# Kernel optimization log

Measured on AMD Instinct MI355X. Metric: run time of the kernel, lower is better.

## Reference

```python
import jax, jax.numpy as jnp
import numpy as np

DIM = 1024
SCALE = 1.0 / np.sqrt(DIM).astype(np.float32)


def setup_inputs() -> dict:
    key = jax.random.key(0)
    ks = jax.random.split(key, 8)
    B, S, D = 4, 2048, DIM
    x = jax.random.normal(ks[0], (B, S, D), dtype=jnp.float32)
    mask = jnp.zeros((S, S), dtype=jnp.float32)  # additive mask, broadcast over batch
    # learned params (nn.Linear: y = x @ W.T + b); store W already transposed for x @ W
    init = 1.0 / np.sqrt(D)
    Wq = jax.random.uniform(ks[1], (D, D), jnp.float32, -init, init)
    bq = jax.random.uniform(ks[2], (D,), jnp.float32, -init, init)
    Wk = jax.random.uniform(ks[3], (D, D), jnp.float32, -init, init)
    bk = jax.random.uniform(ks[4], (D,), jnp.float32, -init, init)
    Wv = jax.random.uniform(ks[5], (D, D), jnp.float32, -init, init)
    bv = jax.random.uniform(ks[6], (D,), jnp.float32, -init, init)
    return {"x": x, "mask": mask, "Wq": Wq, "bq": bq, "Wk": Wk, "bk": bk, "Wv": Wv, "bv": bv}


def reference(x, mask, Wq, bq, Wk, bk, Wv, bv):
    # single-head full-dim attention, scaled by 1/sqrt(dim) (as in the source)
    q = x @ Wq + bq                      # [B, S, D]
    k = x @ Wk + bk                      # [B, S, D]
    v = x @ Wv + bv                      # [B, S, D]
    scores = jnp.einsum('bqd,bkd->bqk', q, k) * SCALE  # [B, S, S]
    scores = scores + mask               # additive mask, broadcast
    attn = jax.nn.softmax(scores, axis=-1)
    # dropout(p=0.1) is identity in eval mode
    return jnp.einsum('bqk,bkd->bqd', attn, v)  # [B, S, D]
```

## Files before the change

### kernel.cpp

```cpp
#include <hip/hip_runtime.h>

typedef unsigned short u16;
typedef unsigned int u32;

typedef __attribute__((ext_vector_type(8))) short bf16x8;
typedef __attribute__((ext_vector_type(4))) float f32x4;

static __device__ __forceinline__ u16 f2bf(float f) {
    u32 u = __float_as_uint(f);
    u32 r = (u + 0x7FFFu + ((u >> 16) & 1u)) >> 16;
    return (u16)r;
}
static __device__ __forceinline__ float bf2f(u16 h) {
    return __uint_as_float(((u32)h) << 16);
}
static __device__ __forceinline__ u32 pack2(float a, float b) {
    return (u32)f2bf(a) | ((u32)f2bf(b) << 16);
}

__global__ __launch_bounds__(256) void convert_bf16_kernel(const float* __restrict__ x,
                                                           u16* __restrict__ y, int n4) {
    int i = blockIdx.x * 256 + threadIdx.x;
    if (i < n4) {
        float4 v = ((const float4*)x)[i];
        ushort4 o;
        o.x = f2bf(v.x); o.y = f2bf(v.y); o.z = f2bf(v.z); o.w = f2bf(v.w);
        ((ushort4*)y)[i] = o;
    }
}

__global__ __launch_bounds__(256) void transpose3_to_bf16_kernel(
    const float* __restrict__ W0, const float* __restrict__ W1, const float* __restrict__ W2,
    u16* __restrict__ T0, u16* __restrict__ T1, u16* __restrict__ T2, int D) {
    __shared__ float t[32][33];
    const float* W = (blockIdx.z == 0) ? W0 : (blockIdx.z == 1) ? W1 : W2;
    u16* WT = (blockIdx.z == 0) ? T0 : (blockIdx.z == 1) ? T1 : T2;
    int bx = blockIdx.x, by = blockIdx.y;
    int tx = threadIdx.x, ty = threadIdx.y;
#pragma unroll
    for (int i = ty; i < 32; i += 8)
        t[i][tx] = W[(long)(by * 32 + i) * D + bx * 32 + tx];
    __syncthreads();
#pragma unroll
    for (int i = ty; i < 32; i += 8)
        WT[(long)(bx * 32 + i) * D + by * 32 + tx] = f2bf(t[tx][i]);
}

__global__ __launch_bounds__(256) void concat_bias_kernel(const float* __restrict__ a,
                                                          const float* __restrict__ b,
                                                          float* __restrict__ o, int n) {
    int i = blockIdx.x * 256 + threadIdx.x;
    if (i < 2 * n) o[i] = (i < n) ? a[i] : b[i - n];
}

__global__ __launch_bounds__(512, 2) void gemm256_kernel(
    const u16* __restrict__ A, int lda, long sA,
    const u16* __restrict__ B, int ldb, long sB,
    void* __restrict__ C, int ldc, long sC, int c_bf16,
    const float* __restrict__ bias, int bias_mode,
    const float* __restrict__ madd, int mask_ld,
    float* __restrict__ rowsum, int rs_mode, int rs_ld,
    float scale, int K) {
    __shared__ __align__(16) u16 SMEM[2][2 * 256 * 64];
    const int bz = blockIdx.z;
    const u16* Ab = A + (long)bz * sA;
    const u16* Bb = B + (long)bz * sB;
    int bx, by;
    {
        const int gx = gridDim.x;
        int flat = blockIdx.y * gx + blockIdx.x;
        const int cpx = (gx * gridDim.y) >> 3;
        flat = (flat & 7) * cpx + (flat >> 3);
        bx = flat % gx;
        by = flat / gx;
    }
    const int tm = by << 8, tn = bx << 8;
    const int tid = threadIdx.x, wave = tid >> 6, lane = tid & 63;
    const int wq = wave & 3;
    const int wm = (wave >> 2) << 7;
    const int wn = wq << 6;
    const int fm = lane & 15, fq = lane >> 4;
    const int T = K >> 6;

    f32x4 acc[8][4];
#pragma unroll
    for (int i = 0; i < 8; i++)
#pragma unroll
        for (int j = 0; j < 4; j++) acc[i][j] = (f32x4){0.f, 0.f, 0.f, 0.f};

    const int srow = tid >> 3;
    const int sslot = tid & 7;

    auto stageA = [&](int t, int half) {
        u16* dst = &SMEM[t & 1][0];
        const int kb = t << 6;
#pragma unroll
        for (int blk = 0; blk < 2; blk++) {
            const int r0 = blk * 128 + half * 64;
            const int r = r0 + srow;
            const int gk = kb + ((sslot ^ (r & 7)) << 3);
            const u16* ga = Ab + (long)(tm + r) * lda + gk;
            __builtin_amdgcn_global_load_lds(
                (const __attribute__((address_space(1))) void*)ga,
                (__attribute__((address_space(3))) void*)&dst[(r0 + wave * 8) * 64], 16, 0, 0);
        }
    };
    auto stageB = [&](int t, int half) {
        u16* dst = &SMEM[t & 1][256 * 64];
        const int kb = t << 6;
#pragma unroll
        for (int blk = 0; blk < 2; blk++) {
            const int r0 = half * 128 + blk * 64;
            const int r = r0 + srow;
            const int g = ((r >> 5) & 3) * 64 + (r >> 7) * 32 + (r & 31);
            const int gk = kb + ((sslot ^ (r & 7)) << 3);
            const u16* gb = Bb + (long)(tn + g) * ldb + gk;
            __builtin_amdgcn_global_load_lds(
                (const __attribute__((address_space(1))) void*)gb,
                (__attribute__((address_space(3))) void*)&dst[(r0 + wave * 8) * 64], 16, 0, 0);
        }
    };

    auto read_a4 = [&](const u16* Ls, bf16x8 (&d)[4][2], int base) {
#pragma unroll
        for (int i = 0; i < 4; i++) {
            const int ra = base + i * 16 + fm;
            const int sw = ra & 7;
#pragma unroll
            for (int kh = 0; kh < 2; kh++)
                d[i][kh] = *(const bf16x8*)&Ls[ra * 64 + (((kh * 4 + fq) ^ sw) << 3)];
        }
    };
    auto read_b2 = [&](const u16* Ls, bf16x8 (&d)[2][2], int base) {
#pragma unroll
        for (int j = 0; j < 2; j++) {
            const int rb = base + j * 16 + fm;
            const int sw = rb & 7;
#pragma unroll
            for (int kh = 0; kh < 2; kh++)
                d[j][kh] = *(const bf16x8*)&Ls[rb * 64 + (((kh * 4 + fq) ^ sw) << 3)];
        }
    };

    stageA(0, 0); stageB(0, 0); stageA(0, 1); stageB(0, 1);
    if (T > 1) {
        stageA(1, 0); stageB(1, 0); stageA(1, 1);
        asm volatile("s_waitcnt vmcnt(6)" ::: "memory");
    } else {
        asm volatile("s_waitcnt vmcnt(0)" ::: "memory");
    }
    __builtin_amdgcn_sched_barrier(0);
    __builtin_amdgcn_s_barrier();
    __builtin_amdgcn_sched_barrier(0);

    bf16x8 alo[4][2], ahi[4][2], blo[2][2], bhi[2][2];
    read_a4(&SMEM[0][0], alo, wm);
    read_b2(&SMEM[0][256 * 64], blo, wq * 32);

    for (int u = 0; u < T; ++u) {
        const u16* As = &SMEM[u & 1][0];
        const u16* Bs = &SMEM[u & 1][256 * 64];
        const u16* As2 = &SMEM[(u + 1) & 1][0];
        const u16* Bs2 = &SMEM[(u + 1) & 1][256 * 64];
        if (u + 1 < T) stageB(u + 1, 1);
        read_b2(Bs, bhi, 128 + wq * 32);
        __builtin_amdgcn_sched_barrier(0);
        __builtin_amdgcn_s_setprio(1);
#pragma unroll
        for (int kh = 0; kh < 2; kh++)
#pragma unroll
            for (int i = 0; i < 4; i++)
#pragma unroll
                for (int j = 0; j < 2; j++)
                    acc[i][j] = __builtin_amdgcn_mfma_f32_16x16x32_bf16(alo[i][kh], blo[j][kh], acc[i][j], 0, 0, 0);
        __builtin_amdgcn_s_setprio(0);
        __builtin_amdgcn_sched_barrier(0);
        __builtin_amdgcn_s_barrier();
        __builtin_amdgcn_sched_barrier(0);
        if (u + 2 < T) stageA(u + 2, 0);
        read_a4(As, ahi, wm + 64);
        __builtin_amdgcn_sched_barrier(0);
        __builtin_amdgcn_s_setprio(1);
#pragma unroll
        for (int kh = 0; kh < 2; kh++)
#pragma unroll
            for (int i = 0; i < 4; i++)
#pragma unroll
                for (int j = 0; j < 2; j++)
                    acc[i][2 + j] = __builtin_amdgcn_mfma_f32_16x16x32_bf16(alo[i][kh], bhi[j][kh], acc[i][2 + j], 0, 0, 0);
        __builtin_amdgcn_s_setprio(0);
        __builtin_amdgcn_sched_barrier(0);
        __builtin_amdgcn_s_barrier();
        __builtin_amdgcn_sched_barrier(0);
        if (u + 2 < T) stageB(u + 2, 0);
        __builtin_amdgcn_sched_barrier(0);
        __builtin_amdgcn_s_setprio(1);
#pragma unroll
        for (int kh = 0; kh < 2; kh++)
#pragma unroll
            for (int i = 0; i < 4; i++)
#pragma unroll
                for (int j = 0; j < 2; j++)
                    acc[4 + i][j] = __builtin_amdgcn_mfma_f32_16x16x32_bf16(ahi[i][kh], blo[j][kh], acc[4 + i][j], 0, 0, 0);
        __builtin_amdgcn_s_setprio(0);
        __builtin_amdgcn_sched_barrier(0);
        __builtin_amdgcn_s_barrier();
        __builtin_amdgcn_sched_barrier(0);
        if (u + 2 < T) {
            stageA(u + 2, 1);
            asm volatile("s_waitcnt vmcnt(6)" ::: "memory");
        } else {
            asm volatile("s_waitcnt vmcnt(0)" ::: "memory");
        }
        __builtin_amdgcn_sched_barrier(0);
        __builtin_amdgcn_s_barrier();
        __builtin_amdgcn_sched_barrier(0);
        if (u + 1 < T) {
            read_a4(As2, alo, wm);
            read_b2(Bs2, blo, wq * 32);
        }
        __builtin_amdgcn_sched_barrier(0);
        __builtin_amdgcn_s_setprio(1);
#pragma unroll
        for (int kh = 0; kh < 2; kh++)
#pragma unroll
            for (int i = 0; i < 4; i++)
#pragma unroll
                for (int j = 0; j < 2; j++)
                    acc[4 + i][2 + j] = __builtin_amdgcn_mfma_f32_16x16x32_bf16(ahi[i][kh], bhi[j][kh], acc[4 + i][2 + j], 0, 0, 0);
        __builtin_amdgcn_s_setprio(0);
    }
    __syncthreads();

    float* EP = (float*)&SMEM[0][0] + wave * 1088;
    const int row16 = lane >> 2, cb = (lane & 3) * 16;
    float4 bc[4];
    if (bias_mode == 1) {
#pragma unroll
        for (int q = 0; q < 4; q++) bc[q] = *(const float4*)&bias[tn + wn + cb + q * 4];
    }
#pragma unroll
    for (int i = 0; i < 8; i++) {
#pragma unroll
        for (int j = 0; j < 4; j++)
#pragma unroll
            for (int r = 0; r < 4; r++)
                EP[(fq * 4 + r) * 68 + j * 16 + fm] = acc[i][j][r];
        const long grow = tm + wm + i * 16 + row16;
        float rb = (bias_mode == 2) ? bias[grow] : 0.f;
        float4 t4[4];
#pragma unroll
        for (int q = 0; q < 4; q++) {
            float4 v = *(const float4*)&EP[row16 * 68 + cb + q * 4];
            v.x = v.x * scale + rb; v.y = v.y * scale + rb;
            v.z = v.z * scale + rb; v.w = v.w * scale + rb;
            if (bias_mode == 1) { v.x += bc[q].x; v.y += bc[q].y; v.z += bc[q].z; v.w += bc[q].w; }
            if (madd) {
                float4 m4 = *(const float4*)&madd[grow * mask_ld + tn + wn + cb + q * 4];
                v.x += m4.x; v.y += m4.y; v.z += m4.z; v.w += m4.w;
            }
            t4[q] = v;
        }
        if (rs_mode == 1) {
            float s = 0.f;
#pragma unroll
            for (int q = 0; q < 4; q++) {
                t4[q].x = __expf(t4[q].x); t4[q].y = __expf(t4[q].y);
                t4[q].z = __expf(t4[q].z); t4[q].w = __expf(t4[q].w);
                s += t4[q].x + t4[q].y + t4[q].z + t4[q].w;
            }
            s += __shfl_xor(s, 1);
            s += __shfl_xor(s, 2);
            if ((lane & 3) == 0) atomicAdd(&rowsum[(long)bz * rs_ld + grow], s);
        } else if (rs_mode == 2) {
            float inv = 1.f / rowsum[(long)bz * rs_ld + grow];
#pragma unroll
            for (int q = 0; q < 4; q++) {
                t4[q].x *= inv; t4[q].y *= inv; t4[q].z *= inv; t4[q].w *= inv;
            }
        }
        if (c_bf16) {
            u16* dst = (u16*)C + (long)bz * sC + grow * ldc + tn + wn + cb;
            uint4 o0 = {pack2(t4[0].x, t4[0].y), pack2(t4[0].z, t4[0].w),
                        pack2(t4[1].x, t4[1].y), pack2(t4[1].z, t4[1].w)};
            uint4 o1 = {pack2(t4[2].x, t4[2].y), pack2(t4[2].z, t4[2].w),
                        pack2(t4[3].x, t4[3].y), pack2(t4[3].z, t4[3].w)};
            *(uint4*)dst = o0;
            *(uint4*)(dst + 8) = o1;
        } else {
            float* dst = (float*)C + (long)bz * sC + grow * ldc + tn + wn + cb;
#pragma unroll
            for (int q = 0; q < 4; q++) *(float4*)(dst + q * 4) = t4[q];
        }
    }
}

__global__ __launch_bounds__(256, 4) void gemm_bt_kernel(
    const u16* __restrict__ A, int lda, long sA,
    const u16* __restrict__ B, int ldb, long sB,
    void* __restrict__ C, int ldc, long sC, int c_bf16,
    const float* __restrict__ bias, int bias_mode,
    const float* __restrict__ madd, int mask_ld,
    float* __restrict__ rowsum, int rs_mode, int rs_ld, int swapxy,
    float scale, int K) {
    __shared__ __align__(16) u16 SMEM[2][256 * 32];
    const int bz = blockIdx.z;
    const u16* Ab = A + (long)bz * sA;
    const u16* Bb = B + (long)bz * sB;
    const int bxi = swapxy ? blockIdx.y : blockIdx.x;
    const int byi = swapxy ? blockIdx.x : blockIdx.y;
    const int tm = byi * 128, tn = bxi * 128;
    const int tid = threadIdx.x, wave = tid >> 6, lane = tid & 63;
    const int wm = (wave >> 1) * 64, wn = (wave & 1) * 64;
    const int lr = lane >> 2, c = lane & 3;
    const int fm = lane & 15, fq = lane >> 4;

    f32x4 acc[4][4];
#pragma unroll
    for (int i = 0; i < 4; i++)
#pragma unroll
        for (int j = 0; j < 4; j++) acc[i][j] = (f32x4){0.f, 0.f, 0.f, 0.f};

    const int T = K >> 5;

    auto stage = [&](int t, int buf) {
        u16* As = &SMEM[buf][0];
        u16* Bs = &SMEM[buf][128 * 32];
#pragma unroll
        for (int r = 0; r < 2; r++) {
            const int rl = r * 64 + wave * 16;
            const int row = rl + lr;
            const int kc = (t << 5) + ((c ^ ((row ^ (row >> 2)) & 3)) << 3);
            const u16* ga = Ab + (long)(tm + row) * lda + kc;
            const u16* gb = Bb + (long)(tn + row) * ldb + kc;
            __builtin_amdgcn_global_load_lds((const __attribute__((address_space(1))) void*)ga,
                                             (__attribute__((address_space(3))) void*)&As[rl * 32],
                                             16, 0, 0);
            __builtin_amdgcn_global_load_lds((const __attribute__((address_space(1))) void*)gb,
                                             (__attribute__((address_space(3))) void*)&Bs[rl * 32],
                                             16, 0, 0);
        }
    };

    stage(0, 0);
    __syncthreads();
    for (int t = 0; t < T; t++) {
        const int cur = t & 1;
        if (t + 1 < T) stage(t + 1, cur ^ 1);
        const u16* As = &SMEM[cur][0];
        const u16* Bs = &SMEM[cur][128 * 32];
        bf16x8 af[4], bfr[4];
#pragma unroll
        for (int i = 0; i < 4; i++) {
            int row = wm + i * 16 + fm;
            af[i] = *(const bf16x8*)&As[row * 32 + ((fq ^ ((row ^ (row >> 2)) & 3)) << 3)];
        }
#pragma unroll
        for (int j = 0; j < 4; j++) {
            int row = wn + j * 16 + fm;
            bfr[j] = *(const bf16x8*)&Bs[row * 32 + ((fq ^ ((row ^ (row >> 2)) & 3)) << 3)];
        }
#pragma unroll
        for (int i = 0; i < 4; i++)
#pragma unroll
            for (int j = 0; j < 4; j++)
                acc[i][j] = __builtin_amdgcn_mfma_f32_16x16x32_bf16(af[i], bfr[j], acc[i][j], 0, 0, 0);
        if (t + 1 < T) __syncthreads();
    }
    __syncthreads();

    float* EP = (float*)&SMEM[0][0] + wave * 1088;
    const int row16 = lane >> 2, cb = (lane & 3) * 16;
    float4 bc[4];
    if (bias_mode == 1) {
#pragma unroll
        for (int q = 0; q < 4; q++) bc[q] = *(const float4*)&bias[tn + wn + cb + q * 4];
    }
#pragma unroll
    for (int i = 0; i < 4; i++) {
#pragma unroll
        for (int j = 0; j < 4; j++)
#pragma unroll
            for (int r = 0; r < 4; r++)
                EP[(fq * 4 + r) * 68 + j * 16 + fm] = acc[i][j][r];
        const long grow = tm + wm + i * 16 + row16;
        float rb = (bias_mode == 2) ? bias[grow] : 0.f;
        float4 t4[4];
#pragma unroll
        for (int q = 0; q < 4; q++) {
            float4 v = *(const float4*)&EP[row16 * 68 + cb + q * 4];
            v.x = v.x * scale + rb; v.y = v.y * scale + rb;
            v.z = v.z * scale + rb; v.w = v.w * scale + rb;
            if (bias_mode == 1) { v.x += bc[q].x; v.y += bc[q].y; v.z += bc[q].z; v.w += bc[q].w; }
            if (madd) {
                float4 m4 = *(const float4*)&madd[grow * mask_ld + tn + wn + cb + q * 4];
                v.x += m4.x; v.y += m4.y; v.z += m4.z; v.w += m4.w;
            }
            t4[q] = v;
        }
        if (rs_mode == 1) {
            float s = 0.f;
#pragma unroll
            for (int q = 0; q < 4; q++) {
                t4[q].x = __expf(t4[q].x); t4[q].y = __expf(t4[q].y);
                t4[q].z = __expf(t4[q].z); t4[q].w = __expf(t4[q].w);
                s += t4[q].x + t4[q].y + t4[q].z + t4[q].w;
            }
            s += __shfl_xor(s, 1);
            s += __shfl_xor(s, 2);
            if ((lane & 3) == 0) atomicAdd(&rowsum[(long)bz * rs_ld + grow], s);
        } else if (rs_mode == 2) {
            float inv = 1.f / rowsum[(long)bz * rs_ld + grow];
#pragma unroll
            for (int q = 0; q < 4; q++) {
                t4[q].x *= inv; t4[q].y *= inv; t4[q].z *= inv; t4[q].w *= inv;
            }
        }
        if (c_bf16) {
            u16* dst = (u16*)C + (long)bz * sC + grow * ldc + tn + wn + cb;
            uint4 o0 = {pack2(t4[0].x, t4[0].y), pack2(t4[0].z, t4[0].w),
                        pack2(t4[1].x, t4[1].y), pack2(t4[1].z, t4[1].w)};
            uint4 o1 = {pack2(t4[2].x, t4[2].y), pack2(t4[2].z, t4[2].w),
                        pack2(t4[3].x, t4[3].y), pack2(t4[3].z, t4[3].w)};
            *(uint4*)dst = o0;
            *(uint4*)(dst + 8) = o1;
        } else {
            float* dst = (float*)C + (long)bz * sC + grow * ldc + tn + wn + cb;
#pragma unroll
            for (int q = 0; q < 4; q++) *(float4*)(dst + q * 4) = t4[q];
        }
    }
}

extern "C" void kernel_launch(void* const* d_in, const int* in_sizes, int n_in,
                              void* d_out, int out_size, void* d_ws, size_t ws_size,
                              hipStream_t stream) {
    const float* x    = (const float*)d_in[0];
    const float* mask = (const float*)d_in[1];
    const float* Wq   = (const float*)d_in[2];
    const float* bq   = (const float*)d_in[3];
    const float* Wk   = (const float*)d_in[4];
    const float* bk   = (const float*)d_in[5];
    const float* Wv   = (const float*)d_in[6];
    const float* bv   = (const float*)d_in[7];
    float* out = (float*)d_out;

    const int B = 4, S = 2048, D = 1024;
    const long MS = (long)B * S;

    size_t need = (size_t)MS * D * 2 + (size_t)(2 * D) * D * 2 + (size_t)D * D * 2
                + (size_t)(2 * D) * 4 + (size_t)MS * (2 * D) * 2 + (size_t)D * MS * 2
                + (size_t)B * S * S * 2 + (size_t)B * S * 4;
    if (ws_size < need) return;

    char* ws = (char*)d_ws;
    u16*  xb   = (u16*)ws;  ws += (long)MS * D * 2;
    u16*  wqkt = (u16*)ws;  ws += (long)(2 * D) * D * 2;
    u16*  wvt  = (u16*)ws;  ws += (long)D * D * 2;
    float* bqk = (float*)ws; ws += (long)(2 * D) * 4;
    u16*  QK   = (u16*)ws;  ws += (long)MS * (2 * D) * 2;
    u16*  VT   = (u16*)ws;  ws += (long)D * MS * 2;
    u16*  sc   = (u16*)ws;  ws += (long)B * S * S * 2;
    float* rsum = (float*)ws; ws += (long)B * S * 4;

    const float SCALE = 0.03125f;

    hipMemsetAsync(rsum, 0, (size_t)B * S * 4, stream);

    convert_bf16_kernel<<<(int)((MS * D / 4 + 255) / 256), 256, 0, stream>>>(x, xb, (int)(MS * D / 4));
    transpose3_to_bf16_kernel<<<dim3(32, 32, 3), dim3(32, 8), 0, stream>>>(
        Wq, Wk, Wv, wqkt, wqkt + (long)D * D, wvt, D);
    concat_bias_kernel<<<8, 256, 0, stream>>>(bq, bk, bqk, D);

    gemm256_kernel<<<dim3(2 * D / 256, (int)(MS / 256), 1), 512, 0, stream>>>(
        xb, D, 0, wqkt, D, 0, QK, 2 * D, 0, 1, bqk, 1, nullptr, 0,
        nullptr, 0, 0, 1.0f, D);
    gemm_bt_kernel<<<dim3((int)(MS / 128), D / 128, 1), 256, 0, stream>>>(
        wvt, D, 0, xb, D, 0, VT, (int)MS, 0, 1, bv, 2, nullptr, 0,
        nullptr, 0, 0, 0, 1.0f, D);

    gemm256_kernel<<<dim3(S / 256, S / 256, B), 512, 0, stream>>>(
        QK, 2 * D, (long)S * 2 * D, QK + D, 2 * D, (long)S * 2 * D, sc, S, (long)S * S, 1,
        nullptr, 0, mask, S, rsum, 1, S, SCALE, D);

    gemm_bt_kernel<<<dim3(S / 128, D / 128, B), 256, 0, stream>>>(
        sc, S, (long)S * S, VT, (int)MS, (long)S, out, D, (long)S * D, 0,
        nullptr, 0, nullptr, 0, rsum, 2, S, 1, 1.0f, S);
}
```

Measured before the change: 279.0 us.

## Store the attention mask as bf16 and remap PV GEMM blocks per XCD

The additive mask is converted once to bf16 in a new small kernel. The score GEMM epilogue then reads half as many mask bytes for each of the four batches. The P·V GEMM grid is reshaped so that blockIdx.x selects the XCD, and each XCD handles one half of one batch, to keep that batch's score rows and V^T in a single L2. The cost is an extra conversion pass over the mask and bf16 rounding of mask values, which changes results for masks that bf16 cannot represent exactly.

```diff
diff --git a/kernel.cpp b/kernel.cpp
--- a/kernel.cpp
+++ b/kernel.cpp
@@ -58,7 +58,7 @@
     const u16* __restrict__ B, int ldb, long sB,
     void* __restrict__ C, int ldc, long sC, int c_bf16,
     const float* __restrict__ bias, int bias_mode,
-    const float* __restrict__ madd, int mask_ld,
+    const u16* __restrict__ madd, int mask_ld,
     float* __restrict__ rowsum, int rs_mode, int rs_ld,
     float scale, int K) {
     __shared__ __align__(16) u16 SMEM[2][2 * 256 * 64];
@@ -256,8 +256,8 @@
             v.z = v.z * scale + rb; v.w = v.w * scale + rb;
             if (bias_mode == 1) { v.x += bc[q].x; v.y += bc[q].y; v.z += bc[q].z; v.w += bc[q].w; }
             if (madd) {
-                float4 m4 = *(const float4*)&madd[grow * mask_ld + tn + wn + cb + q * 4];
-                v.x += m4.x; v.y += m4.y; v.z += m4.z; v.w += m4.w;
+                ushort4 m4 = *(const ushort4*)&madd[grow * mask_ld + tn + wn + cb + q * 4];
+                v.x += bf2f(m4.x); v.y += bf2f(m4.y); v.z += bf2f(m4.z); v.w += bf2f(m4.w);
             }
             t4[q] = v;
         }
@@ -301,14 +301,22 @@
     void* __restrict__ C, int ldc, long sC, int c_bf16,
     const float* __restrict__ bias, int bias_mode,
     const float* __restrict__ madd, int mask_ld,
-    float* __restrict__ rowsum, int rs_mode, int rs_ld, int swapxy,
+    float* __restrict__ rowsum, int rs_mode, int rs_ld, int xcd_mode,
     float scale, int K) {
     __shared__ __align__(16) u16 SMEM[2][256 * 32];
-    const int bz = blockIdx.z;
+    int bxi, byi, bzi;
+    if (xcd_mode == 1) {
+        const int xcd = blockIdx.x;
+        const int s = blockIdx.y + (gridDim.y * blockIdx.z);
+        bzi = xcd >> 1;
+        byi = (xcd & 1) * 8 + (s >> 3);
+        bxi = s & 7;
+    } else {
+        bxi = blockIdx.x; byi = blockIdx.y; bzi = blockIdx.z;
+    }
+    const int bz = bzi;
     const u16* Ab = A + (long)bz * sA;
     const u16* Bb = B + (long)bz * sB;
-    const int bxi = swapxy ? blockIdx.y : blockIdx.x;
-    const int byi = swapxy ? blockIdx.x : blockIdx.y;
     const int tm = byi * 128, tn = bxi * 128;
     const int tid = threadIdx.x, wave = tid >> 6, lane = tid & 63;
     const int wm = (wave >> 1) * 64, wn = (wave & 1) * 64;
@@ -450,7 +458,7 @@
 
     size_t need = (size_t)MS * D * 2 + (size_t)(2 * D) * D * 2 + (size_t)D * D * 2
                 + (size_t)(2 * D) * 4 + (size_t)MS * (2 * D) * 2 + (size_t)D * MS * 2
-                + (size_t)B * S * S * 2 + (size_t)B * S * 4;
+                + (size_t)B * S * S * 2 + (size_t)B * S * 4 + (size_t)S * S * 2;
     if (ws_size < need) return;
 
     char* ws = (char*)d_ws;
@@ -462,12 +470,15 @@
     u16*  VT   = (u16*)ws;  ws += (long)D * MS * 2;
     u16*  sc   = (u16*)ws;  ws += (long)B * S * S * 2;
     float* rsum = (float*)ws; ws += (long)B * S * 4;
+    u16*  maskb = (u16*)ws; ws += (long)S * S * 2;
 
     const float SCALE = 0.03125f;
 
     hipMemsetAsync(rsum, 0, (size_t)B * S * 4, stream);
 
     convert_bf16_kernel<<<(int)((MS * D / 4 + 255) / 256), 256, 0, stream>>>(x, xb, (int)(MS * D / 4));
+    convert_bf16_kernel<<<(int)(((long)S * S / 4 + 255) / 256), 256, 0, stream>>>(
+        mask, maskb, (int)((long)S * S / 4));
     transpose3_to_bf16_kernel<<<dim3(32, 32, 3), dim3(32, 8), 0, stream>>>(
         Wq, Wk, Wv, wqkt, wqkt + (long)D * D, wvt, D);
     concat_bias_kernel<<<8, 256, 0, stream>>>(bq, bk, bqk, D);
@@ -481,9 +492,9 @@
 
     gemm256_kernel<<<dim3(S / 256, S / 256, B), 512, 0, stream>>>(
         QK, 2 * D, (long)S * 2 * D, QK + D, 2 * D, (long)S * 2 * D, sc, S, (long)S * S, 1,
-        nullptr, 0, mask, S, rsum, 1, S, SCALE, D);
-
-    gemm_bt_kernel<<<dim3(S / 128, D / 128, B), 256, 0, stream>>>(
+        nullptr, 0, maskb, S, rsum, 1, S, SCALE, D);
+
+    gemm_bt_kernel<<<dim3(D / 128, S / 128, B), 256, 0, stream>>>(
         sc, S, (long)S * S, VT, (int)MS, (long)S, out, D, (long)S * D, 0,
         nullptr, 0, nullptr, 0, rsum, 2, S, 1, 1.0f, S);
 }
```

New measurement: 281.6 us. No clear change (+0.9%).

## Merge prep and QKV projection launches, bf16 mask, specialize attention GEMMs

Applied to the files above, without the earlier changes.

Folds the x conversion, weight transposes and bias concat into one prep kernel. The Q/K projection and V^T projection run in a single launch that also converts the mask to bf16 and zeroes the row sums, with the QK projection moving from 256-tiles to a shared 128-tile core. The score GEMM now reads the bf16 mask instead of fp32 and drops its runtime mode branches, and the PV GEMM is specialized with an XCD-aware block remap. This cuts launch count and mask traffic, but adds mask rounding to bf16 and a smaller tile for the QK projection.

```diff
diff --git a/kernel.cpp b/kernel.cpp
--- a/kernel.cpp
+++ b/kernel.cpp
@@ -18,48 +18,178 @@
     return (u32)f2bf(a) | ((u32)f2bf(b) << 16);
 }
 
-__global__ __launch_bounds__(256) void convert_bf16_kernel(const float* __restrict__ x,
-                                                           u16* __restrict__ y, int n4) {
-    int i = blockIdx.x * 256 + threadIdx.x;
-    if (i < n4) {
+__global__ __launch_bounds__(256) void prep_kernel(
+    const float* __restrict__ x, u16* __restrict__ xb,
+    const float* __restrict__ Wq, const float* __restrict__ Wk, const float* __restrict__ Wv,
+    u16* __restrict__ T0, u16* __restrict__ T1, u16* __restrict__ T2,
+    const float* __restrict__ bq, const float* __restrict__ bk,
+    float* __restrict__ bqk) {
+    const int D = 1024;
+    int bid = blockIdx.x;
+    const int tid = threadIdx.x;
+    if (bid < 8192) {
+        long i = (long)bid * 256 + tid;
         float4 v = ((const float4*)x)[i];
-        ushort4 o;
-        o.x = f2bf(v.x); o.y = f2bf(v.y); o.z = f2bf(v.z); o.w = f2bf(v.w);
-        ((ushort4*)y)[i] = o;
-    }
-}
-
-__global__ __launch_bounds__(256) void transpose3_to_bf16_kernel(
-    const float* __restrict__ W0, const float* __restrict__ W1, const float* __restrict__ W2,
-    u16* __restrict__ T0, u16* __restrict__ T1, u16* __restrict__ T2, int D) {
-    __shared__ float t[32][33];
-    const float* W = (blockIdx.z == 0) ? W0 : (blockIdx.z == 1) ? W1 : W2;
-    u16* WT = (blockIdx.z == 0) ? T0 : (blockIdx.z == 1) ? T1 : T2;
-    int bx = blockIdx.x, by = blockIdx.y;
-    int tx = threadIdx.x, ty = threadIdx.y;
-#pragma unroll
-    for (int i = ty; i < 32; i += 8)
-        t[i][tx] = W[(long)(by * 32 + i) * D + bx * 32 + tx];
+        ushort4 o; o.x = f2bf(v.x); o.y = f2bf(v.y); o.z = f2bf(v.z); o.w = f2bf(v.w);
+        ((ushort4*)xb)[i] = o;
+        return;
+    }
+    bid -= 8192;
+    if (bid < 3072) {
+        __shared__ float t[32][33];
+        const int z = bid >> 10, loc = bid & 1023;
+        const int bx = loc & 31, by = loc >> 5;
+        const float* W = (z == 0) ? Wq : (z == 1) ? Wk : Wv;
+        u16* WT = (z == 0) ? T0 : (z == 1) ? T1 : T2;
+        const int tx = tid & 31, ty = tid >> 5;
+#pragma unroll
+        for (int i = ty; i < 32; i += 8)
+            t[i][tx] = W[(long)(by * 32 + i) * D + bx * 32 + tx];
+        __syncthreads();
+#pragma unroll
+        for (int i = ty; i < 32; i += 8)
+            WT[(long)(bx * 32 + i) * D + by * 32 + tx] = f2bf(t[tx][i]);
+        return;
+    }
+    bid -= 3072;
+    {
+        int i = bid * 256 + tid;
+        bqk[i] = (i < 1024) ? bq[i] : bk[i - 1024];
+    }
+}
+
+static __device__ __forceinline__ void gemm_core(
+    u16* __restrict__ SM,
+    const u16* __restrict__ Ab, int lda,
+    const u16* __restrict__ Bb, int ldb,
+    void* __restrict__ Cb, int ldc, int c_bf16,
+    const float* __restrict__ bias, int bias_mode,
+    float scale, int K, int tm, int tn) {
+    const int tid = threadIdx.x, wave = tid >> 6, lane = tid & 63;
+    const int wm = (wave >> 1) * 64, wn = (wave & 1) * 64;
+    const int lr = lane >> 2, c = lane & 3;
+    const int fm = lane & 15, fq = lane >> 4;
+
+    f32x4 acc[4][4];
+#pragma unroll
+    for (int i = 0; i < 4; i++)
+#pragma unroll
+        for (int j = 0; j < 4; j++) acc[i][j] = (f32x4){0.f, 0.f, 0.f, 0.f};
+
+    const int T = K >> 5;
+
+    auto stage = [&](int t, int buf) {
+        u16* As = SM + buf * 8192;
+        u16* Bs = As + 4096;
+#pragma unroll
+        for (int r = 0; r < 2; r++) {
+            const int rl = r * 64 + wave * 16;
+            const int row = rl + lr;
+            const int kc = (t << 5) + ((c ^ ((row ^ (row >> 2)) & 3)) << 3);
+            const u16* ga = Ab + (long)(tm + row) * lda + kc;
+            const u16* gb = Bb + (long)(tn + row) * ldb + kc;
+            __builtin_amdgcn_global_load_lds((const __attribute__((address_space(1))) void*)ga,
+                                             (__attribute__((address_space(3))) void*)&As[rl * 32],
+                                             16, 0, 0);
+            __builtin_amdgcn_global_load_lds((const __attribute__((address_space(1))) void*)gb,
+                                             (__attribute__((address_space(3))) void*)&Bs[rl * 32],
+                                             16, 0, 0);
+        }
+    };
+
+    stage(0, 0);
     __syncthreads();
-#pragma unroll
-    for (int i = ty; i < 32; i += 8)
-        WT[(long)(bx * 32 + i) * D + by * 32 + tx] = f2bf(t[tx][i]);
-}
-
-__global__ __launch_bounds__(256) void concat_bias_kernel(const float* __restrict__ a,
-                                                          const float* __restrict__ b,
-                                                          float* __restrict__ o, int n) {
-    int i = blockIdx.x * 256 + threadIdx.x;
-    if (i < 2 * n) o[i] = (i < n) ? a[i] : b[i - n];
+    for (int t = 0; t < T; t++) {
+        const int cur = t & 1;
+        if (t + 1 < T) stage(t + 1, cur ^ 1);
+        const u16* As = SM + cur * 8192;
+        const u16* Bs = As + 4096;
+        bf16x8 af[4], bfr[4];
+#pragma unroll
+        for (int i = 0; i < 4; i++) {
+            int row = wm + i * 16 + fm;
+            af[i] = *(const bf16x8*)&As[row * 32 + ((fq ^ ((row ^ (row >> 2)) & 3)) << 3)];
+        }
+#pragma unroll
+        for (int j = 0; j < 4; j++) {
+            int row = wn + j * 16 + fm;
+            bfr[j] = *(const bf16x8*)&Bs[row * 32 + ((fq ^ ((row ^ (row >> 2)) & 3)) << 3)];
+        }
+#pragma unroll
+        for (int i = 0; i < 4; i++)
+#pragma unroll
+            for (int j = 0; j < 4; j++)
+                acc[i][j] = __builtin_amdgcn_mfma_f32_16x16x32_bf16(af[i], bfr[j], acc[i][j], 0, 0, 0);
+        if (t + 1 < T) __syncthreads();
+    }
+    __syncthreads();
+
+    float* EP = (float*)SM + wave * 1088;
+    const int row16 = lane >> 2, cb = (lane & 3) * 16;
+    float4 bc[4];
+    if (bias_mode == 1) {
+#pragma unroll
+        for (int q = 0; q < 4; q++) bc[q] = *(const float4*)&bias[tn + wn + cb + q * 4];
+    }
+#pragma unroll
+    for (int i = 0; i < 4; i++) {
+#pragma unroll
+        for (int j = 0; j < 4; j++)
+#pragma unroll
+            for (int r = 0; r < 4; r++)
+                EP[(fq * 4 + r) * 68 + j * 16 + fm] = acc[i][j][r];
+        const long grow = tm + wm + i * 16 + row16;
+        float rb = (bias_mode == 2) ? bias[grow] : 0.f;
+        float4 t4[4];
+#pragma unroll
+        for (int q = 0; q < 4; q++) {
+            float4 v = *(const float4*)&EP[row16 * 68 + cb + q * 4];
+            v.x = v.x * scale + rb; v.y = v.y * scale + rb;
+            v.z = v.z * scale + rb; v.w = v.w * scale + rb;
+            if (bias_mode == 1) { v.x += bc[q].x; v.y += bc[q].y; v.z += bc[q].z; v.w += bc[q].w; }
+            t4[q] = v;
+        }
+        u16* dst = (u16*)Cb + grow * ldc + tn + wn + cb;
+        uint4 o0 = {pack2(t4[0].x, t4[0].y), pack2(t4[0].z, t4[0].w),
+                    pack2(t4[1].x, t4[1].y), pack2(t4[1].z, t4[1].w)};
+        uint4 o1 = {pack2(t4[2].x, t4[2].y), pack2(t4[2].z, t4[2].w),
+                    pack2(t4[3].x, t4[3].y), pack2(t4[3].z, t4[3].w)};
+        *(uint4*)dst = o0;
+        *(uint4*)(dst + 8) = o1;
+    }
+}
+
+__global__ __launch_bounds__(256, 4) void gemm_qkvt_kernel(
+    const u16* __restrict__ xb, const u16* __restrict__ wqkt, const u16* __restrict__ wvt,
+    u16* __restrict__ QK, u16* __restrict__ VT,
+    const float* __restrict__ bqk, const float* __restrict__ bv,
+    const float* __restrict__ mask, u16* __restrict__ maskb, float* __restrict__ rsum) {
+    __shared__ __align__(16) u16 SM[2][256 * 32];
+    const int D = 1024, MS = 8192;
+    const int id = blockIdx.x;
+    if (id < 1024) {
+        gemm_core(&SM[0][0], xb, D, wqkt, D, QK, 2 * D, 1, bqk, 1,
+                  1.0f, D, (id >> 4) * 128, (id & 15) * 128);
+    } else if (id < 1536) {
+        const int f = id - 1024;
+        gemm_core(&SM[0][0], wvt, D, xb, D, VT, MS, 1, bv, 2,
+                  1.0f, D, (f >> 6) * 128, (f & 63) * 128);
+    } else if (id < 5632) {
+        long i = (long)(id - 1536) * 256 + threadIdx.x;
+        float4 v = ((const float4*)mask)[i];
+        ushort4 o; o.x = f2bf(v.x); o.y = f2bf(v.y); o.z = f2bf(v.z); o.w = f2bf(v.w);
+        ((ushort4*)maskb)[i] = o;
+    } else {
+        rsum[(id - 5632) * 256 + threadIdx.x] = 0.f;
+    }
 }
 
 __global__ __launch_bounds__(512, 2) void gemm256_kernel(
     const u16* __restrict__ A, int lda, long sA,
     const u16* __restrict__ B, int ldb, long sB,
-    void* __restrict__ C, int ldc, long sC, int c_bf16,
-    const float* __restrict__ bias, int bias_mode,
-    const float* __restrict__ madd, int mask_ld,
-    float* __restrict__ rowsum, int rs_mode, int rs_ld,
+    void* __restrict__ C, int ldc, long sC,
+    const u16* __restrict__ madd, int mask_ld,
+    float* __restrict__ rowsum, int rs_ld,
     float scale, int K) {
     __shared__ __align__(16) u16 SMEM[2][2 * 256 * 64];
     const int bz = blockIdx.z;
@@ -234,11 +364,6 @@
 
     float* EP = (float*)&SMEM[0][0] + wave * 1088;
     const int row16 = lane >> 2, cb = (lane & 3) * 16;
-    float4 bc[4];
-    if (bias_mode == 1) {
-#pragma unroll
-        for (int q = 0; q < 4; q++) bc[q] = *(const float4*)&bias[tn + wn + cb + q * 4];
-    }
 #pragma unroll
     for (int i = 0; i < 8; i++) {
 #pragma unroll
@@ -247,68 +372,48 @@
             for (int r = 0; r < 4; r++)
                 EP[(fq * 4 + r) * 68 + j * 16 + fm] = acc[i][j][r];
         const long grow = tm + wm + i * 16 + row16;
-        float rb = (bias_mode == 2) ? bias[grow] : 0.f;
         float4 t4[4];
 #pragma unroll
         for (int q = 0; q < 4; q++) {
             float4 v = *(const float4*)&EP[row16 * 68 + cb + q * 4];
-            v.x = v.x * scale + rb; v.y = v.y * scale + rb;
-            v.z = v.z * scale + rb; v.w = v.w * scale + rb;
-            if (bias_mode == 1) { v.x += bc[q].x; v.y += bc[q].y; v.z += bc[q].z; v.w += bc[q].w; }
-            if (madd) {
-                float4 m4 = *(const float4*)&madd[grow * mask_ld + tn + wn + cb + q * 4];
-                v.x += m4.x; v.y += m4.y; v.z += m4.z; v.w += m4.w;
-            }
+            ushort4 m4 = *(const ushort4*)&madd[grow * mask_ld + tn + wn + cb + q * 4];
+            v.x = v.x * scale + bf2f(m4.x); v.y = v.y * scale + bf2f(m4.y);
+            v.z = v.z * scale + bf2f(m4.z); v.w = v.w * scale + bf2f(m4.w);
             t4[q] = v;
         }
-        if (rs_mode == 1) {
-            float s = 0.f;
-#pragma unroll
-            for (int q = 0; q < 4; q++) {
-                t4[q].x = __expf(t4[q].x); t4[q].y = __expf(t4[q].y);
-                t4[q].z = __expf(t4[q].z); t4[q].w = __expf(t4[q].w);
-                s += t4[q].x + t4[q].y + t4[q].z + t4[q].w;
-            }
-            s += __shfl_xor(s, 1);
-            s += __shfl_xor(s, 2);
-            if ((lane & 3) == 0) atomicAdd(&rowsum[(long)bz * rs_ld + grow], s);
-        } else if (rs_mode == 2) {
-            float inv = 1.f / rowsum[(long)bz * rs_ld + grow];
-#pragma unroll
-            for (int q = 0; q < 4; q++) {
-                t4[q].x *= inv; t4[q].y *= inv; t4[q].z *= inv; t4[q].w *= inv;
-            }
-        }
-        if (c_bf16) {
-            u16* dst = (u16*)C + (long)bz * sC + grow * ldc + tn + wn + cb;
-            uint4 o0 = {pack2(t4[0].x, t4[0].y), pack2(t4[0].z, t4[0].w),
-                        pack2(t4[1].x, t4[1].y), pack2(t4[1].z, t4[1].w)};
-            uint4 o1 = {pack2(t4[2].x, t4[2].y), pack2(t4[2].z, t4[2].w),
-                        pack2(t4[3].x, t4[3].y), pack2(t4[3].z, t4[3].w)};
-            *(uint4*)dst = o0;
-            *(uint4*)(dst + 8) = o1;
-        } else {
-            float* dst = (float*)C + (long)bz * sC + grow * ldc + tn + wn + cb;
-#pragma unroll
-            for (int q = 0; q < 4; q++) *(float4*)(dst + q * 4) = t4[q];
-        }
-    }
-}
-
-__global__ __launch_bounds__(256, 4) void gemm_bt_kernel(
-    const u16* __restrict__ A, int lda, long sA,
-    const u16* __restrict__ B, int ldb, long sB,
-    void* __restrict__ C, int ldc, long sC, int c_bf16,
-    const float* __restrict__ bias, int bias_mode,
-    const float* __restrict__ madd, int mask_ld,
-    float* __restrict__ rowsum, int rs_mode, int rs_ld, int swapxy,
-    float scale, int K) {
+        float s = 0.f;
+#pragma unroll
+        for (int q = 0; q < 4; q++) {
+            t4[q].x = __expf(t4[q].x); t4[q].y = __expf(t4[q].y);
+            t4[q].z = __expf(t4[q].z); t4[q].w = __expf(t4[q].w);
+            s += t4[q].x + t4[q].y + t4[q].z + t4[q].w;
+        }
+        s += __shfl_xor(s, 1);
+        s += __shfl_xor(s, 2);
+        if ((lane & 3) == 0) atomicAdd(&rowsum[(long)bz * rs_ld + grow], s);
+        u16* dst = (u16*)C + (long)bz * sC + grow * ldc + tn + wn + cb;
+        uint4 o0 = {pack2(t4[0].x, t4[0].y), pack2(t4[0].z, t4[0].w),
+                    pack2(t4[1].x, t4[1].y), pack2(t4[1].z, t4[1].w)};
+        uint4 o1 = {pack2(t4[2].x, t4[2].y), pack2(t4[2].z, t4[2].w),
+                    pack2(t4[3].x, t4[3].y), pack2(t4[3].z, t4[3].w)};
+        *(uint4*)dst = o0;
+        *(uint4*)(dst + 8) = o1;
+    }
+}
+
+__global__ __launch_bounds__(256, 4) void gemm_pv_kernel(
+    const u16* __restrict__ sc, const u16* __restrict__ VT,
+    float* __restrict__ out, const float* __restrict__ rsum) {
     __shared__ __align__(16) u16 SMEM[2][256 * 32];
-    const int bz = blockIdx.z;
-    const u16* Ab = A + (long)bz * sA;
-    const u16* Bb = B + (long)bz * sB;
-    const int bxi = swapxy ? blockIdx.y : blockIdx.x;
-    const int byi = swapxy ? blockIdx.x : blockIdx.y;
+    const int S = 2048, D = 1024, MS = 8192;
+    const int xcd = blockIdx.x;
+    const int s = blockIdx.y + gridDim.y * blockIdx.z;
+    const int bz = xcd >> 1;
+    const int byi = (xcd & 1) * 8 + (s >> 3);
+    const int bxi = s & 7;
+    const u16* Ab = sc + (long)bz * S * S;
+    const u16* Bb = VT + (long)bz * S;
+    const float* rs = rsum + (long)bz * S;
     const int tm = byi * 128, tn = bxi * 128;
     const int tid = threadIdx.x, wave = tid >> 6, lane = tid & 63;
     const int wm = (wave >> 1) * 64, wn = (wave & 1) * 64;
@@ -321,7 +426,7 @@
 #pragma unroll
         for (int j = 0; j < 4; j++) acc[i][j] = (f32x4){0.f, 0.f, 0.f, 0.f};
 
-    const int T = K >> 5;
+    const int T = S >> 5;
 
     auto stage = [&](int t, int buf) {
         u16* As = &SMEM[buf][0];
@@ -331,8 +436,8 @@
             const int rl = r * 64 + wave * 16;
             const int row = rl + lr;
             const int kc = (t << 5) + ((c ^ ((row ^ (row >> 2)) & 3)) << 3);
-            const u16* ga = Ab + (long)(tm + row) * lda + kc;
-            const u16* gb = Bb + (long)(tn + row) * ldb + kc;
+            const u16* ga = Ab + (long)(tm + row) * S + kc;
+            const u16* gb = Bb + (long)(tn + row) * MS + kc;
             __builtin_amdgcn_global_load_lds((const __attribute__((address_space(1))) void*)ga,
                                              (__attribute__((address_space(3))) void*)&As[rl * 32],
                                              16, 0, 0);
@@ -371,11 +476,6 @@
 
     float* EP = (float*)&SMEM[0][0] + wave * 1088;
     const int row16 = lane >> 2, cb = (lane & 3) * 16;
-    float4 bc[4];
-    if (bias_mode == 1) {
-#pragma unroll
-        for (int q = 0; q < 4; q++) bc[q] = *(const float4*)&bias[tn + wn + cb + q * 4];
-    }
 #pragma unroll
     for (int i = 0; i < 4; i++) {
 #pragma unroll
@@ -384,50 +484,13 @@
             for (int r = 0; r < 4; r++)
                 EP[(fq * 4 + r) * 68 + j * 16 + fm] = acc[i][j][r];
         const long grow = tm + wm + i * 16 + row16;
-        float rb = (bias_mode == 2) ? bias[grow] : 0.f;
-        float4 t4[4];
+        float inv = 1.f / rs[grow];
+        float* dst = out + (long)bz * S * D + grow * D + tn + wn + cb;
 #pragma unroll
         for (int q = 0; q < 4; q++) {
             float4 v = *(const float4*)&EP[row16 * 68 + cb + q * 4];
-            v.x = v.x * scale + rb; v.y = v.y * scale + rb;
-            v.z = v.z * scale + rb; v.w = v.w * scale + rb;
-            if (bias_mode == 1) { v.x += bc[q].x; v.y += bc[q].y; v.z += bc[q].z; v.w += bc[q].w; }
-            if (madd) {
-                float4 m4 = *(const float4*)&madd[grow * mask_ld + tn + wn + cb + q * 4];
-                v.x += m4.x; v.y += m4.y; v.z += m4.z; v.w += m4.w;
-            }
-            t4[q] = v;
-        }
-        if (rs_mode == 1) {
-            float s = 0.f;
-#pragma unroll
-            for (int q = 0; q < 4; q++) {
-                t4[q].x = __expf(t4[q].x); t4[q].y = __expf(t4[q].y);
-                t4[q].z = __expf(t4[q].z); t4[q].w = __expf(t4[q].w);
-                s += t4[q].x + t4[q].y + t4[q].z + t4[q].w;
-            }
-            s += __shfl_xor(s, 1);
-            s += __shfl_xor(s, 2);
-            if ((lane & 3) == 0) atomicAdd(&rowsum[(long)bz * rs_ld + grow], s);
-        } else if (rs_mode == 2) {
-            float inv = 1.f / rowsum[(long)bz * rs_ld + grow];
-#pragma unroll
-            for (int q = 0; q < 4; q++) {
-                t4[q].x *= inv; t4[q].y *= inv; t4[q].z *= inv; t4[q].w *= inv;
-            }
-        }
-        if (c_bf16) {
-            u16* dst = (u16*)C + (long)bz * sC + grow * ldc + tn + wn + cb;
-            uint4 o0 = {pack2(t4[0].x, t4[0].y), pack2(t4[0].z, t4[0].w),
-                        pack2(t4[1].x, t4[1].y), pack2(t4[1].z, t4[1].w)};
-            uint4 o1 = {pack2(t4[2].x, t4[2].y), pack2(t4[2].z, t4[2].w),
-                        pack2(t4[3].x, t4[3].y), pack2(t4[3].z, t4[3].w)};
-            *(uint4*)dst = o0;
-            *(uint4*)(dst + 8) = o1;
-        } else {
-            float* dst = (float*)C + (long)bz * sC + grow * ldc + tn + wn + cb;
-#pragma unroll
-            for (int q = 0; q < 4; q++) *(float4*)(dst + q * 4) = t4[q];
+            v.x *= inv; v.y *= inv; v.z *= inv; v.w *= inv;
+            *(float4*)(dst + q * 4) = v;
         }
     }
 }
@@ -450,7 +513,7 @@
 
     size_t need = (size_t)MS * D * 2 + (size_t)(2 * D) * D * 2 + (size_t)D * D * 2
                 + (size_t)(2 * D) * 4 + (size_t)MS * (2 * D) * 2 + (size_t)D * MS * 2
-                + (size_t)B * S * S * 2 + (size_t)B * S * 4;
+                + (size_t)B * S * S * 2 + (size_t)B * S * 4 + (size_t)S * S * 2;
     if (ws_size < need) return;
 
     char* ws = (char*)d_ws;
@@ -462,28 +525,16 @@
     u16*  VT   = (u16*)ws;  ws += (long)D * MS * 2;
     u16*  sc   = (u16*)ws;  ws += (long)B * S * S * 2;
     float* rsum = (float*)ws; ws += (long)B * S * 4;
+    u16*  maskb = (u16*)ws; ws += (long)S * S * 2;
 
     const float SCALE = 0.03125f;
 
-    hipMemsetAsync(rsum, 0, (size_t)B * S * 4, stream);
-
-    convert_bf16_kernel<<<(int)((MS * D / 4 + 255) / 256), 256, 0, stream>>>(x, xb, (int)(MS * D / 4));
-    transpose3_to_bf16_kernel<<<dim3(32, 32, 3), dim3(32, 8), 0, stream>>>(
-        Wq, Wk, Wv, wqkt, wqkt + (long)D * D, wvt, D);
-    concat_bias_kernel<<<8, 256, 0, stream>>>(bq, bk, bqk, D);
-
-    gemm256_kernel<<<dim3(2 * D / 256, (int)(MS / 256), 1), 512, 0, stream>>>(
-        xb, D, 0, wqkt, D, 0, QK, 2 * D, 0, 1, bqk, 1, nullptr, 0,
-        nullptr, 0, 0, 1.0f, D);
-    gemm_bt_kernel<<<dim3((int)(MS / 128), D / 128, 1), 256, 0, stream>>>(
-        wvt, D, 0, xb, D, 0, VT, (int)MS, 0, 1, bv, 2, nullptr, 0,
-        nullptr, 0, 0, 0, 1.0f, D);
-
+    prep_kernel<<<11272, 256, 0, stream>>>(x, xb, Wq, Wk, Wv,
+                                           wqkt, wqkt + (long)D * D, wvt, bq, bk, bqk);
+    gemm_qkvt_kernel<<<5664, 256, 0, stream>>>(xb, wqkt, wvt, QK, VT, bqk, bv,
+                                               mask, maskb, rsum);
     gemm256_kernel<<<dim3(S / 256, S / 256, B), 512, 0, stream>>>(
-        QK, 2 * D, (long)S * 2 * D, QK + D, 2 * D, (long)S * 2 * D, sc, S, (long)S * S, 1,
-        nullptr, 0, mask, S, rsum, 1, S, SCALE, D);
-
-    gemm_bt_kernel<<<dim3(S / 128, D / 128, B), 256, 0, stream>>>(
-        sc, S, (long)S * S, VT, (int)MS, (long)S, out, D, (long)S * D, 0,
-        nullptr, 0, nullptr, 0, rsum, 2, S, 1, 1.0f, S);
-}
+        QK, 2 * D, (long)S * 2 * D, QK + D, 2 * D, (long)S * 2 * D, sc, S, (long)S * S,
+        maskb, S, rsum, S, SCALE, D);
+    gemm_pv_kernel<<<dim3(8, 16, 4), 256, 0, stream>>>(sc, VT, out, rsum);
+}
```

After: 263.2 us, median of 2. 1.06x faster.
